# Performance work log

Measured on AMD Instinct MI355X. Metric: run time of the kernel, lower is better.

The kernel has to match this reference:

```python
import jax, jax.numpy as jnp
import numpy as np

ORDER = 3  # truncation level; num_components = ORDER*(ORDER+1)//2 = 6 (independent weights)


def setup_inputs() -> dict:
    key = jax.random.key(0)
    k1, k2, k3 = jax.random.split(key, 3)
    B, T, D, F = 64, 4096, 128, 64
    C = ORDER * (ORDER + 1) // 2
    sequences = jax.random.normal(k1, (B, T, D), dtype=jnp.float32)
    # ls2t_uniform-style init: scaled uniform per component
    kernel = jax.random.normal(k2, (C, D, F), dtype=jnp.float32) / np.sqrt(D)
    bias = jax.random.normal(k3, (C, F), dtype=jnp.float32) * 0.01
    return {"sequences": sequences, "kernel": kernel, "bias": bias}


def _exclusive_cumsum(x, axis):
    # exclusive cumsum = inclusive cumsum minus self (avoids concat/pad allocs)
    return jnp.cumsum(x, axis=axis) - x


def reference(sequences, kernel, bias):
    # sequences: [B, T, D]; kernel: [C, D, F]; bias: [C, F]
    # M[c] = sequences @ kernel[c] + bias[c]  -> [C, B, T, F]
    M = jnp.einsum('btd,cdf->cbtf', sequences, kernel) + bias[:, None, None, :]
    # Level 1: plain sum over time of first component
    Y = [jnp.sum(M[0], axis=1)]  # [B, F]
    k = 1
    for m in range(1, ORDER):
        R = M[k]
        k += 1
        for _ in range(m):
            # iterated-sum recursion: strictly-lower-triangular (exclusive) cumsum over time
            R = M[k] * _exclusive_cumsum(R, axis=1)
            k += 1
        Y.append(jnp.sum(R, axis=1))
    return jnp.stack(Y, axis=-1)  # [B, F, ORDER]
```

## Files before the change

kernel.cpp:

```cpp
#include <hip/hip_runtime.h>
#include <hip/hip_bf16.h>


#define B_ 64
#define T_ 4096
#define D_ 128
#define F_ 64
#define TB 512
#define TGROUPS (T_ / TB)
#define CHT 32
#define NITER (TB / CHT)
#define TPB 512
#define RING 3

typedef __attribute__((ext_vector_type(8))) short short8v;
typedef __attribute__((ext_vector_type(4))) float f32x4;

__device__ __forceinline__ unsigned short bfb(float x) {
    __hip_bfloat16 h = __float2bfloat16(x);
    unsigned short u;
    __builtin_memcpy(&u, &h, 2);
    return u;
}

#define BAR() asm volatile("s_waitcnt lgkmcnt(0)\n\ts_barrier" ::: "memory")
#define VW(n) asm volatile("s_waitcnt vmcnt(" #n ")" ::: "memory")

__global__ __launch_bounds__(TPB)
void ls2t_kernel(const float* __restrict__ seq,
                 const float* __restrict__ kern,
                 const float* __restrict__ bias,
                 float* __restrict__ ws)
{
    __shared__ float slds[RING][CHT * D_];

    const int tid  = threadIdx.x;
    const int tg   = blockIdx.x;
    const int b    = blockIdx.y;
    const int lane = tid & 63;
    const int w    = tid >> 6;
    const int cg   = w >> 2;
    const int wv   = w & 3;
    const int fr   = lane & 15;
    const int lg   = lane >> 4;
    const int f    = wv * 16 + fr;

    short8v bfrag[3][4];
    float bc[3];
    #pragma unroll
    for (int cc = 0; cc < 3; ++cc) {
        const int c = cg * 3 + cc;
        bc[cc] = bias[c * F_ + f];
        #pragma unroll
        for (int ks = 0; ks < 4; ++ks) {
            const float* kp = kern + ((size_t)c * D_ + ks * 32 + lg * 8) * F_ + f;
            short8v bf;
            #pragma unroll
            for (int j = 0; j < 8; ++j) bf[j] = (short)bfb(kp[(size_t)j * F_]);
            bfrag[cc][ks] = bf;
        }
    }

    const float* sbase = seq + ((size_t)b * T_ + (size_t)tg * TB) * D_;

    const int u_lane = lane & 31;
    const float* gsrc0[2];
    #pragma unroll
    for (int j = 0; j < 2; ++j) {
        const int r  = 4 * w + 2 * j + (lane >> 5);
        const int gu = (u_lane & 24) | ((u_lane ^ r) & 7);
        const int t0 = ((r & 15) >> 2) * 128 + ((r >> 4) << 2) + (r & 3);
        gsrc0[j] = sbase + (size_t)t0 * D_ + gu * 4;
    }

    auto issue = [&](int i, int bufi) {
        #pragma unroll
        for (int j = 0; j < 2; ++j) {
            const float* src = gsrc0[j] + (size_t)i * 8 * D_;
            void* dst = (void*)&slds[bufi][(4 * w + 2 * j) * 128];
            __builtin_amdgcn_global_load_lds(
                (const __attribute__((address_space(1))) void*)src,
                (__attribute__((address_space(3))) void*)dst, 16, 0, 0);
        }
    };

    float x0 = 0.f, x1 = 0.f, x2 = 0.f, x3 = 0.f, x4 = 0.f, x5 = 0.f;

    auto compute = [&](int bufi) {
        const float* L = &slds[bufi][0];
        #pragma unroll
        for (int tf = 0; tf < 2; ++tf) {
            f32x4 acc[3];
            #pragma unroll
            for (int cc = 0; cc < 3; ++cc)
                acc[cc] = (f32x4){bc[cc], bc[cc], bc[cc], bc[cc]};

            const int rowbase = (tf * 16 + fr) * 128;
            #pragma unroll
            for (int ks = 0; ks < 4; ++ks) {
                const int u0  = ks * 8 + lg * 2;
                const int s0  = (u0 & 24) | ((u0 ^ fr) & 7);
                const int s1u = ((u0 + 1) & 24) | (((u0 + 1) ^ fr) & 7);
                float4 fa = *reinterpret_cast<const float4*>(&L[rowbase + s0 * 4]);
                float4 fb = *reinterpret_cast<const float4*>(&L[rowbase + s1u * 4]);
                uint4 pk;
                pk.x = __builtin_amdgcn_perm(__float_as_uint(fa.y),
                                             __float_as_uint(fa.x), 0x07060302u);
                pk.y = __builtin_amdgcn_perm(__float_as_uint(fa.w),
                                             __float_as_uint(fa.z), 0x07060302u);
                pk.z = __builtin_amdgcn_perm(__float_as_uint(fb.y),
                                             __float_as_uint(fb.x), 0x07060302u);
                pk.w = __builtin_amdgcn_perm(__float_as_uint(fb.w),
                                             __float_as_uint(fb.z), 0x07060302u);
                short8v a = *reinterpret_cast<short8v*>(&pk);
                #pragma unroll
                for (int cc = 0; cc < 3; ++cc)
                    acc[cc] = __builtin_amdgcn_mfma_f32_16x16x32_bf16(
                        a, bfrag[cc][ks], acc[cc], 0, 0, 0);
            }

            #pragma unroll
            for (int r = 0; r < 4; ++r) {
                float p = acc[0][r], q = acc[1][r], rr = acc[2][r];
                x5 = fmaf(rr, x3, x5);
                x4 = fmaf(rr, x1, x4);
                x3 = fmaf(q,  x0, x3);
                x2 += rr;
                x1 += q;
                x0 += p;
            }
        }
    };

    issue(0, 0); issue(1, 1);

    int b0 = 0, b1 = 1, b2 = 2;
    #pragma unroll 1
    for (int i = 0; i < NITER - 2; ++i) {
        VW(2);
        BAR();
        issue(i + 2, b2);
        compute(b0);
        int t = b0; b0 = b1; b1 = b2; b2 = t;
    }
    VW(2); BAR(); compute(b0);
    VW(0); BAR(); compute(b1);

    #pragma unroll
    for (int m = 16; m <= 32; m <<= 1) {
        float o0 = __shfl_xor(x0, m), o1 = __shfl_xor(x1, m);
        float o2 = __shfl_xor(x2, m), o3 = __shfl_xor(x3, m);
        float o4 = __shfl_xor(x4, m), o5 = __shfl_xor(x5, m);
        const bool up = (lane & m) != 0;
        float A0 = up ? o0 : x0, B0 = up ? x0 : o0;
        float A1 = up ? o1 : x1, B1 = up ? x1 : o1;
        float A2 = up ? o2 : x2, B2 = up ? x2 : o2;
        float A3 = up ? o3 : x3, B3 = up ? x3 : o3;
        float A4 = up ? o4 : x4, B4 = up ? x4 : o4;
        float A5 = up ? o5 : x5, B5 = up ? x5 : o5;
        x5 = A5 + B5 + A3 * B2 + A0 * B4;
        x4 = A4 + B4 + A1 * B2;
        x3 = A3 + B3 + A0 * B1;
        x2 = A2 + B2;
        x1 = A1 + B1;
        x0 = A0 + B0;
    }

    if (lg == 0) {
        float* wp = ws + (((size_t)b * TGROUPS + tg) * F_ + f) * 10;
        if (cg == 0) {
            wp[0] = x0; wp[1] = x1; wp[2] = x2; wp[3] = x4;
        } else {
            wp[4] = x0; wp[5] = x1; wp[6] = x2;
            wp[7] = x3; wp[8] = x4; wp[9] = x5;
        }
    }
}

struct St { float a0, s1, s2, q2, su, sv, sw, qvu, qwv, qwvu; };

__device__ __forceinline__ St mergeSt(const St& A, const St& B) {
    St r;
    r.a0   = A.a0 + B.a0;
    r.q2   = A.q2 + B.q2 + A.s1 * B.s2;
    r.s1   = A.s1 + B.s1;
    r.s2   = A.s2 + B.s2;
    r.qwvu = A.qwvu + B.qwvu + A.qvu * B.sw + A.su * B.qwv;
    r.qwv  = A.qwv + B.qwv + A.sv * B.sw;
    r.qvu  = A.qvu + B.qvu + A.su * B.sv;
    r.su   = A.su + B.su;
    r.sv   = A.sv + B.sv;
    r.sw   = A.sw + B.sw;
    return r;
}

__global__ __launch_bounds__(64)
void ls2t_fold_kernel(const float* __restrict__ ws, float* __restrict__ out)
{
    const int b = blockIdx.x;
    const int f = threadIdx.x;
    St A = {0, 0, 0, 0, 0, 0, 0, 0, 0, 0};
    #pragma unroll
    for (int g = 0; g < TGROUPS; ++g) {
        const float* rp = ws + (((size_t)b * TGROUPS + g) * F_ + f) * 10;
        St r = {rp[0], rp[1], rp[2], rp[3], rp[4],
                rp[5], rp[6], rp[7], rp[8], rp[9]};
        A = mergeSt(A, r);
    }
    float* op = out + ((size_t)b * F_ + f) * 3;
    op[0] = A.a0;
    op[1] = A.q2;
    op[2] = A.qwvu;
}

extern "C" void kernel_launch(void* const* d_in, const int* in_sizes, int n_in,
                              void* d_out, int out_size, void* d_ws, size_t ws_size,
                              hipStream_t stream) {
    const float* seq  = (const float*)d_in[0];
    const float* kern = (const float*)d_in[1];
    const float* bias = (const float*)d_in[2];
    float* out = (float*)d_out;
    float* ws  = (float*)d_ws;

    dim3 g1(TGROUPS, B_);
    ls2t_kernel<<<g1, TPB, 0, stream>>>(seq, kern, bias, ws);
    ls2t_fold_kernel<<<B_, F_, 0, stream>>>(ws, out);
}
```

Baseline: 41.55 us.

## Convert fp32 tile to bf16 once in shared staging buffer before MFMA

Adds a double-buffered bf16 LDS staging area. The block converts each fp32 chunk once, writing it in a swizzled layout, and the MFMA loop then reads ready-made bf16 fragments with one 16-byte load. Before this, every wave reread the fp32 tile and repeated the pack/perm conversion. That duplicated LDS reads and VALU work across the eight waves. In exchange the pipeline gains a convert stage, and LDS use grows, which can limit blocks per CU.

```diff
diff --git a/kernel.cpp b/kernel.cpp
--- a/kernel.cpp
+++ b/kernel.cpp
@@ -11,7 +11,8 @@
 #define CHT 32
 #define NITER (TB / CHT)
 #define TPB 512
-#define RING 3
+#define RINGF 3
+#define RINGH 2
 
 typedef __attribute__((ext_vector_type(8))) short short8v;
 typedef __attribute__((ext_vector_type(4))) float f32x4;
@@ -32,7 +33,8 @@
                  const float* __restrict__ bias,
                  float* __restrict__ ws)
 {
-    __shared__ float slds[RING][CHT * D_];
+    __shared__ float slds[RINGF][CHT * D_];
+    __shared__ unsigned short hlds[RINGH][CHT * D_];
 
     const int tid  = threadIdx.x;
     const int tg   = blockIdx.x;
@@ -84,10 +86,32 @@
         }
     };
 
+    auto convert = [&](int fbuf, int hbuf) {
+        const int row = tid >> 4;
+        const int u   = tid & 15;
+        const float* Fp = &slds[fbuf][0];
+        const int v0 = 2 * u, v1 = 2 * u + 1;
+        const int p0 = (v0 & 24) | ((v0 ^ row) & 7);
+        const int p1 = (v1 & 24) | ((v1 ^ row) & 7);
+        float4 fa = *reinterpret_cast<const float4*>(&Fp[row * 128 + p0 * 4]);
+        float4 fb = *reinterpret_cast<const float4*>(&Fp[row * 128 + p1 * 4]);
+        uint4 pk;
+        pk.x = __builtin_amdgcn_perm(__float_as_uint(fa.y),
+                                     __float_as_uint(fa.x), 0x07060302u);
+        pk.y = __builtin_amdgcn_perm(__float_as_uint(fa.w),
+                                     __float_as_uint(fa.z), 0x07060302u);
+        pk.z = __builtin_amdgcn_perm(__float_as_uint(fb.y),
+                                     __float_as_uint(fb.x), 0x07060302u);
+        pk.w = __builtin_amdgcn_perm(__float_as_uint(fb.w),
+                                     __float_as_uint(fb.z), 0x07060302u);
+        *reinterpret_cast<uint4*>(
+            &hlds[hbuf][row * 128 + ((u ^ (row & 15)) * 8)]) = pk;
+    };
+
     float x0 = 0.f, x1 = 0.f, x2 = 0.f, x3 = 0.f, x4 = 0.f, x5 = 0.f;
 
-    auto compute = [&](int bufi) {
-        const float* L = &slds[bufi][0];
+    auto compute = [&](int hbuf) {
+        const unsigned short* H = &hlds[hbuf][0];
         #pragma unroll
         for (int tf = 0; tf < 2; ++tf) {
             f32x4 acc[3];
@@ -98,21 +122,9 @@
             const int rowbase = (tf * 16 + fr) * 128;
             #pragma unroll
             for (int ks = 0; ks < 4; ++ks) {
-                const int u0  = ks * 8 + lg * 2;
-                const int s0  = (u0 & 24) | ((u0 ^ fr) & 7);
-                const int s1u = ((u0 + 1) & 24) | (((u0 + 1) ^ fr) & 7);
-                float4 fa = *reinterpret_cast<const float4*>(&L[rowbase + s0 * 4]);
-                float4 fb = *reinterpret_cast<const float4*>(&L[rowbase + s1u * 4]);
-                uint4 pk;
-                pk.x = __builtin_amdgcn_perm(__float_as_uint(fa.y),
-                                             __float_as_uint(fa.x), 0x07060302u);
-                pk.y = __builtin_amdgcn_perm(__float_as_uint(fa.w),
-                                             __float_as_uint(fa.z), 0x07060302u);
-                pk.z = __builtin_amdgcn_perm(__float_as_uint(fb.y),
-                                             __float_as_uint(fb.x), 0x07060302u);
-                pk.w = __builtin_amdgcn_perm(__float_as_uint(fb.w),
-                                             __float_as_uint(fb.z), 0x07060302u);
-                short8v a = *reinterpret_cast<short8v*>(&pk);
+                const int u = (ks * 4 + lg) ^ fr;
+                short8v a = *reinterpret_cast<const short8v*>(
+                    &H[rowbase + u * 8]);
                 #pragma unroll
                 for (int cc = 0; cc < 3; ++cc)
                     acc[cc] = __builtin_amdgcn_mfma_f32_16x16x32_bf16(
@@ -133,18 +145,28 @@
     };
 
     issue(0, 0); issue(1, 1);
-
-    int b0 = 0, b1 = 1, b2 = 2;
+    int c0 = 0, c1 = 1, c2 = 2;
+
+    VW(2); BAR();
+    issue(2, c2);
+    convert(c0, 0);
+    { int t = c0; c0 = c1; c1 = c2; c2 = t; }
+
     #pragma unroll 1
-    for (int i = 0; i < NITER - 2; ++i) {
+    for (int i = 1; i < NITER - 1; ++i) {
         VW(2);
         BAR();
-        issue(i + 2, b2);
-        compute(b0);
-        int t = b0; b0 = b1; b1 = b2; b2 = t;
-    }
-    VW(2); BAR(); compute(b0);
-    VW(0); BAR(); compute(b1);
+        if (i + 2 < NITER) issue(i + 2, c2);
+        compute((i - 1) & 1);
+        convert(c0, i & 1);
+        int t = c0; c0 = c1; c1 = c2; c2 = t;
+    }
+
+    VW(0); BAR();
+    compute(0);
+    convert(c0, 1);
+    BAR();
+    compute(1);
 
     #pragma unroll
     for (int m = 16; m <= 32; m <<= 1) {
```

Result: no change. 41.55 us (-0.0%).
